# Kernel optimization log

Hardware: AMD Instinct MI355X
Metric: run time of the kernel (lower is better)

Reference implementation:

```python
import jax, jax.numpy as jnp
import numpy as np

B, S, D, H = 4, 2048, 1024, 16
DH = D // H


def setup_inputs() -> dict:
    key = jax.random.key(0)
    ks = jax.random.split(key, 5)
    scale = 0.02
    return {
        "in_features": jax.random.normal(ks[0], (B, S, D), dtype=jnp.float32),
        "Wq": jax.random.normal(ks[1], (D, D), dtype=jnp.float32) * scale,
        "Wk": jax.random.normal(ks[2], (D, D), dtype=jnp.float32) * scale,
        "Wv": jax.random.normal(ks[3], (D, D), dtype=jnp.float32) * scale,
        "Wo": jax.random.normal(ks[4], (D, D), dtype=jnp.float32) * scale,
    }


def reference(in_features, Wq, Wk, Wv, Wo):
    x = in_features  # [B, S, D]
    # projections: einsum '... s d_in, d_model d_in -> ... s d_model'  == x @ W.T
    q = jnp.einsum('bsd,md->bsm', x, Wq)
    k = jnp.einsum('bsd,md->bsm', x, Wk)
    v = jnp.einsum('bsd,md->bsm', x, Wv)
    # split heads: [B, H, S, DH]
    q = q.reshape(B, S, H, DH).transpose(0, 2, 1, 3)
    k = k.reshape(B, S, H, DH).transpose(0, 2, 1, 3)
    v = v.reshape(B, S, H, DH).transpose(0, 2, 1, 3)
    scale = 1.0 / jnp.sqrt(jnp.asarray(DH, dtype=q.dtype))
    scores = jnp.einsum('bhqd,bhkd->bhqk', q, k) * scale  # [B, H, S, S]
    causal = jnp.tril(jnp.ones((S, S), dtype=bool))
    scores = jnp.where(causal[None, None, :, :], scores, -jnp.inf)
    attn = jax.nn.softmax(scores, axis=-1)
    out = jnp.einsum('bhqk,bhkd->bhqd', attn, v)  # [B, H, S, DH]
    out = out.transpose(0, 2, 1, 3).reshape(B, S, D)
    # output projection: einsum '... s d_v, d_model d_v -> ... s d_model' == out @ Wo.T
    return jnp.einsum('bsd,md->bsm', out, Wo)
```

## Files before the change

kernel.cpp:

```cpp
#include <hip/hip_runtime.h>

typedef unsigned short u16;
typedef unsigned int u32;
typedef __attribute__((ext_vector_type(8))) short bf16x8;
typedef __attribute__((ext_vector_type(4))) short bf16x4;
typedef __attribute__((ext_vector_type(4))) float f32x4;

#define S_LEN 2048
#define NHEAD 16
#define DHEAD 64
#define DMODEL 1024

__device__ __forceinline__ u16 f2bf(float f) {
  unsigned u = __builtin_bit_cast(unsigned, f);
  unsigned r = (u + 0x7fffu + ((u >> 16) & 1u)) >> 16;
  return (u16)r;
}

__device__ __forceinline__ void gld_lds16(const void* g, void* l) {
  __builtin_amdgcn_global_load_lds((const __attribute__((address_space(1))) unsigned*)g,
                                   (__attribute__((address_space(3))) unsigned*)l,
                                   16, 0, 0);
}

__global__ void cast_all_kernel(const float* __restrict__ x,
                                const float* __restrict__ Wq, const float* __restrict__ Wk,
                                const float* __restrict__ Wv, const float* __restrict__ Wo,
                                u16* __restrict__ out) {
  int id = blockIdx.x * 256 + threadIdx.x;
  const float* s;
  int j;
  if (id < 2097152) {
    s = x; j = id;
  } else {
    int wid = id - 2097152;
    int wsel = wid >> 18;
    j = wid & 262143;
    s = wsel < 2 ? (wsel == 0 ? Wq : Wk) : (wsel == 2 ? Wv : Wo);
  }
  float4 v = reinterpret_cast<const float4*>(s)[j];
  ushort4 o;
  o.x = f2bf(v.x); o.y = f2bf(v.y); o.z = f2bf(v.z); o.w = f2bf(v.w);
  reinterpret_cast<ushort4*>(out)[id] = o;
}

__global__ __launch_bounds__(256) void gemm_qkv(const u16* __restrict__ A, const u16* __restrict__ Bw,
                                                u16* __restrict__ Qb) {
  __shared__ u16 smem[17408];
  u16* lA = smem;
  u16* lB = smem + 8192;
  const int hw = blockIdx.x;
  const int xcd = hw & 7, vv = hw >> 3;
  const int by = xcd * 8 + (vv & 7);
  const int bx = vv >> 3;
  const int tid = threadIdx.x;
  const int w = tid >> 6, lane = tid & 63;
  const int wm = w >> 1, wn = w & 1;
  const int c = lane & 15, qr = lane >> 4;
  const int brow = by * 128, bcol = bx * 128;
  const int sw = (qr ^ ((c >> 1) & 3)) * 8;
  f32x4 acc[4][4];
#pragma unroll
  for (int m = 0; m < 4; ++m)
#pragma unroll
    for (int n = 0; n < 4; ++n) acc[m][n] = (f32x4){0.f, 0.f, 0.f, 0.f};

  auto stage = [&](int kt, int bsel) {
    const int k0 = kt * 32;
#pragma unroll
    for (int i = 0; i < 2; ++i) {
      int slot = i * 256 + w * 64 + lane;
      int r = slot >> 2, sg = slot & 3;
      int sgs = sg ^ ((r >> 1) & 3);
      gld_lds16(A + (size_t)(brow + r) * DMODEL + k0 + sgs * 8, lA + bsel * 4096 + (i * 256 + w * 64) * 8);
      gld_lds16(Bw + (size_t)(bcol + r) * DMODEL + k0 + sgs * 8, lB + bsel * 4096 + (i * 256 + w * 64) * 8);
    }
  };

  stage(0, 0);
  __syncthreads();
  int cur = 0;
  for (int kt = 0; kt < 32; ++kt) {
    if (kt < 31) stage(kt + 1, cur ^ 1);
    bf16x8 af[4], bfr[4];
#pragma unroll
    for (int m = 0; m < 4; ++m) af[m] = *(const bf16x8*)(lA + cur * 4096 + (wm * 64 + m * 16 + c) * 32 + sw);
#pragma unroll
    for (int n = 0; n < 4; ++n) bfr[n] = *(const bf16x8*)(lB + cur * 4096 + (wn * 64 + n * 16 + c) * 32 + sw);
    __builtin_amdgcn_s_setprio(1);
#pragma unroll
    for (int m = 0; m < 4; ++m)
#pragma unroll
      for (int n = 0; n < 4; ++n)
        acc[m][n] = __builtin_amdgcn_mfma_f32_16x16x32_bf16(af[m], bfr[n], acc[m][n], 0, 0, 0);
    __builtin_amdgcn_s_setprio(0);
    __syncthreads();
    cur ^= 1;
  }

  u16* Kb = Qb + 8388608;
  u16* Vt = Kb + 8388608;
  const int mat = bcol >> 10;
  const int batch = by >> 4;
  const int sbase = brow & 2047;
  const int hbase = (bcol & 1023) >> 6;
  u16* ep = smem;

  if (mat == 2) {
#pragma unroll
    for (int mt = 0; mt < 4; ++mt)
#pragma unroll
      for (int nt = 0; nt < 4; ++nt) {
        int n = wn * 64 + nt * 16 + c;
        int m0 = wm * 64 + mt * 16 + qr * 4;
        ushort4 pk;
        pk.x = f2bf(acc[mt][nt][0]); pk.y = f2bf(acc[mt][nt][1]);
        pk.z = f2bf(acc[mt][nt][2]); pk.w = f2bf(acc[mt][nt][3]);
        *reinterpret_cast<ushort4*>(ep + n * 136 + m0) = pk;
      }
    __syncthreads();
#pragma unroll
    for (int i = 0; i < 8; ++i) {
      int id = i * 256 + tid;
      int n = id >> 4, mch = id & 15;
      int head = hbase + (n >> 6), dh = n & 63;
      uint4 v4 = *reinterpret_cast<const uint4*>(ep + n * 136 + mch * 8);
      *reinterpret_cast<uint4*>(Vt + ((size_t)(batch * NHEAD + head) * DHEAD + dh) * S_LEN + sbase + mch * 8) = v4;
    }
  } else {
    float scale = (mat == 0) ? 0.1803368801111204f : 1.0f;
    u16* dst = (mat == 0) ? Qb : Kb;
#pragma unroll
    for (int mt = 0; mt < 4; ++mt)
#pragma unroll
      for (int nt = 0; nt < 4; ++nt) {
        int n = wn * 64 + nt * 16 + c;
        int m0 = wm * 64 + mt * 16 + qr * 4;
#pragma unroll
        for (int r = 0; r < 4; ++r)
          ep[(m0 + r) * 136 + n] = f2bf(acc[mt][nt][r] * scale);
      }
    __syncthreads();
#pragma unroll
    for (int i = 0; i < 8; ++i) {
      int id = i * 256 + tid;
      int m = id >> 4, hh = (id >> 3) & 1, ch = id & 7;
      int head = hbase + hh;
      int s = sbase + m;
      uint4 v4 = *reinterpret_cast<const uint4*>(ep + m * 136 + hh * 64 + ch * 8);
      *reinterpret_cast<uint4*>(dst + ((size_t)(batch * NHEAD + head) * S_LEN + s) * DHEAD + ch * 8) = v4;
    }
  }
}

__global__ __launch_bounds__(256) void gemm_bt(const u16* __restrict__ A, const u16* __restrict__ Bw,
                                               float* __restrict__ outp) {
  __shared__ u16 lA[2][128 * 32];
  __shared__ u16 lB[2][128 * 32];
  const int hw = blockIdx.x;
  const int xcd = hw & 7, vv = hw >> 3;
  const int bx = vv >> 3, by = xcd * 8 + (vv & 7);
  const int tid = threadIdx.x;
  const int w = tid >> 6, lane = tid & 63;
  const int wm = w >> 1, wn = w & 1;
  const int c = lane & 15, qr = lane >> 4;
  const int brow = by * 128, bcol = bx * 128;
  const int sw = (qr ^ ((c >> 1) & 3)) * 8;
  f32x4 acc[4][4];
#pragma unroll
  for (int m = 0; m < 4; ++m)
#pragma unroll
    for (int n = 0; n < 4; ++n) acc[m][n] = (f32x4){0.f, 0.f, 0.f, 0.f};

  auto stage = [&](int kt, int bsel) {
    const int k0 = kt * 32;
#pragma unroll
    for (int i = 0; i < 2; ++i) {
      int slot = i * 256 + w * 64 + lane;
      int r = slot >> 2, sg = slot & 3;
      int sgs = sg ^ ((r >> 1) & 3);
      gld_lds16(A + (size_t)(brow + r) * DMODEL + k0 + sgs * 8, &lA[bsel][(i * 256 + w * 64) * 8]);
      gld_lds16(Bw + (size_t)(bcol + r) * DMODEL + k0 + sgs * 8, &lB[bsel][(i * 256 + w * 64) * 8]);
    }
  };

  stage(0, 0);
  __syncthreads();
  int cur = 0;
  for (int kt = 0; kt < 32; ++kt) {
    if (kt < 31) stage(kt + 1, cur ^ 1);
    bf16x8 af[4], bfr[4];
#pragma unroll
    for (int m = 0; m < 4; ++m) af[m] = *(const bf16x8*)(&lA[cur][(wm * 64 + m * 16 + c) * 32 + sw]);
#pragma unroll
    for (int n = 0; n < 4; ++n) bfr[n] = *(const bf16x8*)(&lB[cur][(wn * 64 + n * 16 + c) * 32 + sw]);
    __builtin_amdgcn_s_setprio(1);
#pragma unroll
    for (int m = 0; m < 4; ++m)
#pragma unroll
      for (int n = 0; n < 4; ++n)
        acc[m][n] = __builtin_amdgcn_mfma_f32_16x16x32_bf16(af[m], bfr[n], acc[m][n], 0, 0, 0);
    __builtin_amdgcn_s_setprio(0);
    __syncthreads();
    cur ^= 1;
  }

  const int rb = qr * 4;
#pragma unroll
  for (int m = 0; m < 4; ++m)
#pragma unroll
    for (int n = 0; n < 4; ++n) {
      f32x4 a = acc[m][n];
      int gm0 = brow + wm * 64 + m * 16 + rb;
      int gn = bcol + wn * 64 + n * 16 + c;
#pragma unroll
      for (int r = 0; r < 4; ++r) outp[(size_t)(gm0 + r) * DMODEL + gn] = a[r];
    }
}

__global__ __launch_bounds__(512, 4) void attn_kernel(const u16* __restrict__ Q, const u16* __restrict__ K,
                                                      const u16* __restrict__ Vt, u16* __restrict__ O) {
  __shared__ u16 lsK[2][64 * 64];
  __shared__ u16 lsV[2][64 * 64];
  __shared__ u16 lsP[8][16 * 64];
  const int x = blockIdx.x;
  const int xcd = x & 7, v = x >> 3;
  const int by = xcd * 8 + (v & 7);
  const int g = 15 - (v >> 3);
  const int tid = threadIdx.x;
  const int w = tid >> 6, lane = tid & 63;
  const int c = lane & 15, qr = lane >> 4;
  const int b = by >> 4, h = by & 15;
  u16* lp = lsP[w];

  const int q0 = g * 128 + w * 16;
  const int nd = 2 * g + (w >> 2);
  const int ntiles = 2 * g + 2;

  const u16* qrow = Q + ((size_t)by * S_LEN + q0 + c) * DHEAD;
  const bf16x8 aQ0 = *(const bf16x8*)(qrow + qr * 8);
  const bf16x8 aQ1 = *(const bf16x8*)(qrow + 32 + qr * 8);

  f32x4 o_acc[4];
#pragma unroll
  for (int d = 0; d < 4; ++d) o_acc[d] = (f32x4){0.f, 0.f, 0.f, 0.f};
  float l_run = 0.f;

  auto stage = [&](int kt, int bsel) {
    const int kv0 = kt * 64;
    int r = tid >> 3, p = tid & 7;
    int ps = p ^ (r & 7);
    gld_lds16(K + ((size_t)by * S_LEN + kv0 + r) * DHEAD + ps * 8, &lsK[bsel][(w * 64) * 8]);
    gld_lds16(Vt + ((size_t)by * DHEAD + r) * S_LEN + kv0 + ps * 8, &lsV[bsel][(w * 64) * 8]);
  };

  auto process = [&](const u16* bK, const u16* bV, int kt) {
    const int kv0 = kt * 64;
    f32x4 sc[4];
    __builtin_amdgcn_s_setprio(1);
#pragma unroll
    for (int nt = 0; nt < 4; ++nt) {
      int row = nt * 16 + c;
      const bf16x8 k0 = *(const bf16x8*)(bK + row * 64 + ((qr ^ (row & 7)) * 8));
      const bf16x8 k1 = *(const bf16x8*)(bK + row * 64 + (((4 + qr) ^ (row & 7)) * 8));
      f32x4 z = (f32x4){0.f, 0.f, 0.f, 0.f};
      z = __builtin_amdgcn_mfma_f32_16x16x32_bf16(k0, aQ0, z, 0, 0, 0);
      z = __builtin_amdgcn_mfma_f32_16x16x32_bf16(k1, aQ1, z, 0, 0, 0);
      sc[nt] = z;
    }
    __builtin_amdgcn_s_setprio(0);

    if (kt == nd) {
#pragma unroll
      for (int nt = 0; nt < 4; ++nt)
#pragma unroll
        for (int r = 0; r < 4; ++r) {
          int k_g = kv0 + nt * 16 + qr * 4 + r;
          int q_g = q0 + c;
          if (k_g > q_g) sc[nt][r] = -1e30f;
        }
    }

    float rs = 0.f;
#pragma unroll
    for (int nt = 0; nt < 4; ++nt) {
      float p0 = __builtin_amdgcn_exp2f(sc[nt][0]);
      float p1 = __builtin_amdgcn_exp2f(sc[nt][1]);
      float p2 = __builtin_amdgcn_exp2f(sc[nt][2]);
      float p3 = __builtin_amdgcn_exp2f(sc[nt][3]);
      rs += (p0 + p1) + (p2 + p3);
      u32 w01 = __builtin_amdgcn_perm(__builtin_bit_cast(u32, p1), __builtin_bit_cast(u32, p0), 0x07060302u);
      u32 w23 = __builtin_amdgcn_perm(__builtin_bit_cast(u32, p3), __builtin_bit_cast(u32, p2), 0x07060302u);
      uint2 pk; pk.x = w01; pk.y = w23;
      *reinterpret_cast<uint2*>(lp + c * 64 + (((nt * 4 + qr) ^ c) * 4)) = pk;
    }
    l_run += rs;

    bf16x8 pb[2];
#pragma unroll
    for (int ks = 0; ks < 2; ++ks) {
      bf16x4 lo = *(const bf16x4*)(lp + c * 64 + (((ks * 8 + qr * 2) ^ c) * 4));
      bf16x4 hi = *(const bf16x4*)(lp + c * 64 + (((ks * 8 + qr * 2 + 1) ^ c) * 4));
      pb[ks] = (bf16x8){lo[0], lo[1], lo[2], lo[3], hi[0], hi[1], hi[2], hi[3]};
    }
    __builtin_amdgcn_s_setprio(1);
#pragma unroll
    for (int dt = 0; dt < 4; ++dt) {
      int rowv = dt * 16 + c;
#pragma unroll
      for (int ks = 0; ks < 2; ++ks) {
        const bf16x8 vb = *(const bf16x8*)(bV + rowv * 64 + (((ks * 4 + qr) ^ (rowv & 7)) * 8));
        o_acc[dt] = __builtin_amdgcn_mfma_f32_16x16x32_bf16(vb, pb[ks], o_acc[dt], 0, 0, 0);
      }
    }
    __builtin_amdgcn_s_setprio(0);
  };

  stage(0, 0);
  __syncthreads();
  for (int kt = 0; kt < ntiles; kt += 2) {
    if (kt + 1 < ntiles) stage(kt + 1, 1);
    if (kt <= nd) process(lsK[0], lsV[0], kt);
    __syncthreads();
    if (kt + 2 < ntiles) stage(kt + 2, 0);
    if (kt + 1 <= nd) process(lsK[1], lsV[1], kt + 1);
    __syncthreads();
  }

  {
    l_run += __shfl_xor(l_run, 16);
    l_run += __shfl_xor(l_run, 32);
    float rl = 1.0f / l_run;
    int s = q0 + c;
#pragma unroll
    for (int dt = 0; dt < 4; ++dt) {
      ushort4 ok;
#pragma unroll
      for (int r = 0; r < 4; ++r) ((u16*)&ok)[r] = f2bf(o_acc[dt][r] * rl);
      *reinterpret_cast<ushort4*>(O + (((size_t)b * S_LEN + s) * NHEAD + h) * DHEAD + dt * 16 + qr * 4) = ok;
    }
  }
}

extern "C" void kernel_launch(void* const* d_in, const int* in_sizes, int n_in,
                              void* d_out, int out_size, void* d_ws, size_t ws_size,
                              hipStream_t stream) {
  (void)in_sizes; (void)n_in; (void)out_size; (void)ws_size;
  const float* x  = (const float*)d_in[0];
  const float* Wq = (const float*)d_in[1];
  const float* Wk = (const float*)d_in[2];
  const float* Wv = (const float*)d_in[3];
  const float* Wo = (const float*)d_in[4];

  u16* ws  = (u16*)d_ws;
  u16* xb  = ws;
  u16* wqb = xb  + 8388608;
  u16* wob = wqb + 3145728;
  u16* Qb  = wqb + 4194304;
  u16* Kb  = Qb  + 8388608;
  u16* Vt  = Kb  + 8388608;
  u16* Ob  = Vt  + 8388608;

  cast_all_kernel<<<12288, 256, 0, stream>>>(x, Wq, Wk, Wv, Wo, xb);

  gemm_qkv<<<1536, 256, 0, stream>>>(xb, wqb, Qb);
  attn_kernel<<<1024, 512, 0, stream>>>(Qb, Kb, Vt, Ob);
  gemm_bt<<<512, 256, 0, stream>>>(Ob, wob, (float*)d_out);
}
```

Baseline: 163.2 us.

## Process two query subtiles per wave in attention to reuse K/V fragments

Each attention wave now handles 32 query rows, as two 16-row subtiles, instead of 16, so each block covers 256 queries and the grid is halved. The K and V fragments read from LDS are reused across both subtiles, and the staged K/V tiles serve twice as many queries, which cuts LDS and global traffic per unit of work. The block-to-query-tile mapping is reordered for causal load balance. The cost is more registers per wave (accumulators, Q fragments and P buffers double), fewer blocks for load balancing, and a larger P LDS buffer, all of which may reduce occupancy.

```diff
diff --git a/kernel.cpp b/kernel.cpp
--- a/kernel.cpp
+++ b/kernel.cpp
@@ -222,95 +222,115 @@
                                                       const u16* __restrict__ Vt, u16* __restrict__ O) {
   __shared__ u16 lsK[2][64 * 64];
   __shared__ u16 lsV[2][64 * 64];
-  __shared__ u16 lsP[8][16 * 64];
+  __shared__ u16 lsP[8][2][16 * 64];
   const int x = blockIdx.x;
   const int xcd = x & 7, v = x >> 3;
   const int by = xcd * 8 + (v & 7);
-  const int g = 15 - (v >> 3);
+  const int p = v >> 3;
+  const int g = (p < 4) ? (7 - p) : (p - 4);
   const int tid = threadIdx.x;
   const int w = tid >> 6, lane = tid & 63;
   const int c = lane & 15, qr = lane >> 4;
   const int b = by >> 4, h = by & 15;
-  u16* lp = lsP[w];
-
-  const int q0 = g * 128 + w * 16;
-  const int nd = 2 * g + (w >> 2);
-  const int ntiles = 2 * g + 2;
-
-  const u16* qrow = Q + ((size_t)by * S_LEN + q0 + c) * DHEAD;
-  const bf16x8 aQ0 = *(const bf16x8*)(qrow + qr * 8);
-  const bf16x8 aQ1 = *(const bf16x8*)(qrow + 32 + qr * 8);
-
-  f32x4 o_acc[4];
-#pragma unroll
-  for (int d = 0; d < 4; ++d) o_acc[d] = (f32x4){0.f, 0.f, 0.f, 0.f};
-  float l_run = 0.f;
+
+  const int q0 = g * 256 + w * 32;
+  const int nd = 4 * g + (w >> 1);
+  const int ntiles = 4 * g + 4;
+
+  bf16x8 aQ[2][2];
+#pragma unroll
+  for (int qt = 0; qt < 2; ++qt)
+#pragma unroll
+    for (int ks = 0; ks < 2; ++ks)
+      aQ[qt][ks] = *(const bf16x8*)(Q + ((size_t)by * S_LEN + q0 + qt * 16 + c) * DHEAD + ks * 32 + qr * 8);
+
+  f32x4 o_acc[2][4];
+#pragma unroll
+  for (int qt = 0; qt < 2; ++qt)
+#pragma unroll
+    for (int d = 0; d < 4; ++d) o_acc[qt][d] = (f32x4){0.f, 0.f, 0.f, 0.f};
+  float l_run[2] = {0.f, 0.f};
 
   auto stage = [&](int kt, int bsel) {
     const int kv0 = kt * 64;
-    int r = tid >> 3, p = tid & 7;
-    int ps = p ^ (r & 7);
+    int r = tid >> 3, pp = tid & 7;
+    int ps = pp ^ (r & 7);
     gld_lds16(K + ((size_t)by * S_LEN + kv0 + r) * DHEAD + ps * 8, &lsK[bsel][(w * 64) * 8]);
     gld_lds16(Vt + ((size_t)by * DHEAD + r) * S_LEN + kv0 + ps * 8, &lsV[bsel][(w * 64) * 8]);
   };
 
   auto process = [&](const u16* bK, const u16* bV, int kt) {
     const int kv0 = kt * 64;
-    f32x4 sc[4];
+    f32x4 sc2[2][4];
     __builtin_amdgcn_s_setprio(1);
 #pragma unroll
     for (int nt = 0; nt < 4; ++nt) {
       int row = nt * 16 + c;
       const bf16x8 k0 = *(const bf16x8*)(bK + row * 64 + ((qr ^ (row & 7)) * 8));
       const bf16x8 k1 = *(const bf16x8*)(bK + row * 64 + (((4 + qr) ^ (row & 7)) * 8));
-      f32x4 z = (f32x4){0.f, 0.f, 0.f, 0.f};
-      z = __builtin_amdgcn_mfma_f32_16x16x32_bf16(k0, aQ0, z, 0, 0, 0);
-      z = __builtin_amdgcn_mfma_f32_16x16x32_bf16(k1, aQ1, z, 0, 0, 0);
-      sc[nt] = z;
+#pragma unroll
+      for (int qt = 0; qt < 2; ++qt) {
+        f32x4 z = (f32x4){0.f, 0.f, 0.f, 0.f};
+        z = __builtin_amdgcn_mfma_f32_16x16x32_bf16(k0, aQ[qt][0], z, 0, 0, 0);
+        z = __builtin_amdgcn_mfma_f32_16x16x32_bf16(k1, aQ[qt][1], z, 0, 0, 0);
+        sc2[qt][nt] = z;
+      }
     }
     __builtin_amdgcn_s_setprio(0);
 
     if (kt == nd) {
 #pragma unroll
-      for (int nt = 0; nt < 4; ++nt)
-#pragma unroll
-        for (int r = 0; r < 4; ++r) {
-          int k_g = kv0 + nt * 16 + qr * 4 + r;
-          int q_g = q0 + c;
-          if (k_g > q_g) sc[nt][r] = -1e30f;
-        }
-    }
-
-    float rs = 0.f;
-#pragma unroll
-    for (int nt = 0; nt < 4; ++nt) {
-      float p0 = __builtin_amdgcn_exp2f(sc[nt][0]);
-      float p1 = __builtin_amdgcn_exp2f(sc[nt][1]);
-      float p2 = __builtin_amdgcn_exp2f(sc[nt][2]);
-      float p3 = __builtin_amdgcn_exp2f(sc[nt][3]);
-      rs += (p0 + p1) + (p2 + p3);
-      u32 w01 = __builtin_amdgcn_perm(__builtin_bit_cast(u32, p1), __builtin_bit_cast(u32, p0), 0x07060302u);
-      u32 w23 = __builtin_amdgcn_perm(__builtin_bit_cast(u32, p3), __builtin_bit_cast(u32, p2), 0x07060302u);
-      uint2 pk; pk.x = w01; pk.y = w23;
-      *reinterpret_cast<uint2*>(lp + c * 64 + (((nt * 4 + qr) ^ c) * 4)) = pk;
-    }
-    l_run += rs;
-
-    bf16x8 pb[2];
-#pragma unroll
-    for (int ks = 0; ks < 2; ++ks) {
-      bf16x4 lo = *(const bf16x4*)(lp + c * 64 + (((ks * 8 + qr * 2) ^ c) * 4));
-      bf16x4 hi = *(const bf16x4*)(lp + c * 64 + (((ks * 8 + qr * 2 + 1) ^ c) * 4));
-      pb[ks] = (bf16x8){lo[0], lo[1], lo[2], lo[3], hi[0], hi[1], hi[2], hi[3]};
+      for (int qt = 0; qt < 2; ++qt)
+#pragma unroll
+        for (int nt = 0; nt < 4; ++nt)
+#pragma unroll
+          for (int r = 0; r < 4; ++r) {
+            int k_g = kv0 + nt * 16 + qr * 4 + r;
+            int q_g = q0 + qt * 16 + c;
+            if (k_g > q_g) sc2[qt][nt][r] = -1e30f;
+          }
+    }
+
+#pragma unroll
+    for (int qt = 0; qt < 2; ++qt) {
+      u16* lp = lsP[w][qt];
+      float rs = 0.f;
+#pragma unroll
+      for (int nt = 0; nt < 4; ++nt) {
+        float p0 = __builtin_amdgcn_exp2f(sc2[qt][nt][0]);
+        float p1 = __builtin_amdgcn_exp2f(sc2[qt][nt][1]);
+        float p2 = __builtin_amdgcn_exp2f(sc2[qt][nt][2]);
+        float p3 = __builtin_amdgcn_exp2f(sc2[qt][nt][3]);
+        rs += (p0 + p1) + (p2 + p3);
+        u32 w01 = __builtin_amdgcn_perm(__builtin_bit_cast(u32, p1), __builtin_bit_cast(u32, p0), 0x07060302u);
+        u32 w23 = __builtin_amdgcn_perm(__builtin_bit_cast(u32, p3), __builtin_bit_cast(u32, p2), 0x07060302u);
+        uint2 pk; pk.x = w01; pk.y = w23;
+        *reinterpret_cast<uint2*>(lp + c * 64 + (((nt * 4 + qr) ^ c) * 4)) = pk;
+      }
+      l_run[qt] += rs;
+    }
+
+    bf16x8 pb[2][2];
+#pragma unroll
+    for (int qt = 0; qt < 2; ++qt) {
+      u16* lp = lsP[w][qt];
+#pragma unroll
+      for (int ks = 0; ks < 2; ++ks) {
+        bf16x4 lo = *(const bf16x4*)(lp + c * 64 + (((ks * 8 + qr * 2) ^ c) * 4));
+        bf16x4 hi = *(const bf16x4*)(lp + c * 64 + (((ks * 8 + qr * 2 + 1) ^ c) * 4));
+        pb[qt][ks] = (bf16x8){lo[0], lo[1], lo[2], lo[3], hi[0], hi[1], hi[2], hi[3]};
+      }
     }
     __builtin_amdgcn_s_setprio(1);
 #pragma unroll
     for (int dt = 0; dt < 4; ++dt) {
       int rowv = dt * 16 + c;
-#pragma unroll
-      for (int ks = 0; ks < 2; ++ks) {
-        const bf16x8 vb = *(const bf16x8*)(bV + rowv * 64 + (((ks * 4 + qr) ^ (rowv & 7)) * 8));
-        o_acc[dt] = __builtin_amdgcn_mfma_f32_16x16x32_bf16(vb, pb[ks], o_acc[dt], 0, 0, 0);
+      const bf16x8 v0 = *(const bf16x8*)(bV + rowv * 64 + ((qr ^ (rowv & 7)) * 8));
+      const bf16x8 v1 = *(const bf16x8*)(bV + rowv * 64 + (((4 + qr) ^ (rowv & 7)) * 8));
+#pragma unroll
+      for (int qt = 0; qt < 2; ++qt) {
+        o_acc[qt][dt] = __builtin_amdgcn_mfma_f32_16x16x32_bf16(v0, pb[qt][0], o_acc[qt][dt], 0, 0, 0);
+        o_acc[qt][dt] = __builtin_amdgcn_mfma_f32_16x16x32_bf16(v1, pb[qt][1], o_acc[qt][dt], 0, 0, 0);
       }
     }
     __builtin_amdgcn_s_setprio(0);
@@ -327,16 +347,18 @@
     __syncthreads();
   }
 
-  {
-    l_run += __shfl_xor(l_run, 16);
-    l_run += __shfl_xor(l_run, 32);
-    float rl = 1.0f / l_run;
-    int s = q0 + c;
+#pragma unroll
+  for (int qt = 0; qt < 2; ++qt) {
+    float lr = l_run[qt];
+    lr += __shfl_xor(lr, 16);
+    lr += __shfl_xor(lr, 32);
+    float rl = 1.0f / lr;
+    int s = q0 + qt * 16 + c;
 #pragma unroll
     for (int dt = 0; dt < 4; ++dt) {
       ushort4 ok;
 #pragma unroll
-      for (int r = 0; r < 4; ++r) ((u16*)&ok)[r] = f2bf(o_acc[dt][r] * rl);
+      for (int r = 0; r < 4; ++r) ((u16*)&ok)[r] = f2bf(o_acc[qt][dt][r] * rl);
       *reinterpret_cast<ushort4*>(O + (((size_t)b * S_LEN + s) * NHEAD + h) * DHEAD + dt * 16 + qr * 4) = ok;
     }
   }
@@ -364,6 +386,6 @@
   cast_all_kernel<<<12288, 256, 0, stream>>>(x, Wq, Wk, Wv, Wo, xb);
 
   gemm_qkv<<<1536, 256, 0, stream>>>(xb, wqb, Qb);
-  attn_kernel<<<1024, 512, 0, stream>>>(Qb, Kb, Vt, Ob);
+  attn_kernel<<<512, 512, 0, stream>>>(Qb, Kb, Vt, Ob);
   gemm_bt<<<512, 256, 0, stream>>>(Ob, wob, (float*)d_out);
 }
```

New measurement: 168.7 us. +3.4%, slower.

## Triple-buffer K/V tiles and overlap next QK^T with current softmax-PV

Applied to the files above, without the earlier changes.

Splits the attention tile step into a QK^T stage and a softmax+PV stage, with K/V tiles kept in three shared-memory buffers. Each iteration computes the next tile's scores while finishing the current tile's softmax and PV, so there is one barrier per tile. The aim is to hide MFMA latency and exp/LDS work behind each other and keep loads two tiles ahead. In exchange, LDS per block grows by about a third and the carried score registers add register pressure, which may cut occupancy.

```diff
diff --git a/kernel.cpp b/kernel.cpp
--- a/kernel.cpp
+++ b/kernel.cpp
@@ -220,8 +220,8 @@
 
 __global__ __launch_bounds__(512, 4) void attn_kernel(const u16* __restrict__ Q, const u16* __restrict__ K,
                                                       const u16* __restrict__ Vt, u16* __restrict__ O) {
-  __shared__ u16 lsK[2][64 * 64];
-  __shared__ u16 lsV[2][64 * 64];
+  __shared__ u16 lsK[3][64 * 64];
+  __shared__ u16 lsV[3][64 * 64];
   __shared__ u16 lsP[8][16 * 64];
   const int x = blockIdx.x;
   const int xcd = x & 7, v = x >> 3;
@@ -246,17 +246,15 @@
   for (int d = 0; d < 4; ++d) o_acc[d] = (f32x4){0.f, 0.f, 0.f, 0.f};
   float l_run = 0.f;
 
-  auto stage = [&](int kt, int bsel) {
+  auto stage = [&](int kt, u16* dK, u16* dV) {
     const int kv0 = kt * 64;
     int r = tid >> 3, p = tid & 7;
     int ps = p ^ (r & 7);
-    gld_lds16(K + ((size_t)by * S_LEN + kv0 + r) * DHEAD + ps * 8, &lsK[bsel][(w * 64) * 8]);
-    gld_lds16(Vt + ((size_t)by * DHEAD + r) * S_LEN + kv0 + ps * 8, &lsV[bsel][(w * 64) * 8]);
-  };
-
-  auto process = [&](const u16* bK, const u16* bV, int kt) {
-    const int kv0 = kt * 64;
-    f32x4 sc[4];
+    gld_lds16(K + ((size_t)by * S_LEN + kv0 + r) * DHEAD + ps * 8, dK + (w * 64) * 8);
+    gld_lds16(Vt + ((size_t)by * DHEAD + r) * S_LEN + kv0 + ps * 8, dV + (w * 64) * 8);
+  };
+
+  auto qk = [&](const u16* bK, f32x4* sc) {
     __builtin_amdgcn_s_setprio(1);
 #pragma unroll
     for (int nt = 0; nt < 4; ++nt) {
@@ -269,7 +267,10 @@
       sc[nt] = z;
     }
     __builtin_amdgcn_s_setprio(0);
-
+  };
+
+  auto smpv = [&](const u16* bV, f32x4* sc, int kt) {
+    const int kv0 = kt * 64;
     if (kt == nd) {
 #pragma unroll
       for (int nt = 0; nt < 4; ++nt)
@@ -280,7 +281,6 @@
           if (k_g > q_g) sc[nt][r] = -1e30f;
         }
     }
-
     float rs = 0.f;
 #pragma unroll
     for (int nt = 0; nt < 4; ++nt) {
@@ -316,15 +316,25 @@
     __builtin_amdgcn_s_setprio(0);
   };
 
-  stage(0, 0);
+  u16 *K0 = lsK[0], *K1 = lsK[1], *K2 = lsK[2];
+  u16 *V0 = lsV[0], *V1 = lsV[1], *V2 = lsV[2];
+  f32x4 scA[4], scB[4];
+
+  stage(0, K0, V0);
+  stage(1, K1, V1);
   __syncthreads();
-  for (int kt = 0; kt < ntiles; kt += 2) {
-    if (kt + 1 < ntiles) stage(kt + 1, 1);
-    if (kt <= nd) process(lsK[0], lsV[0], kt);
-    __syncthreads();
-    if (kt + 2 < ntiles) stage(kt + 2, 0);
-    if (kt + 1 <= nd) process(lsK[1], lsV[1], kt + 1);
-    __syncthreads();
+  qk(K0, scA);
+
+#pragma unroll 1
+  for (int t = 0; t < ntiles; ++t) {
+    if (t + 2 < ntiles) stage(t + 2, K2, V2);
+    if (t + 1 <= nd) qk(K1, scB);
+    if (t <= nd) smpv(V0, scA, t);
+    __syncthreads();
+    u16* tk = K0; K0 = K1; K1 = K2; K2 = tk;
+    u16* tv = V0; V0 = V1; V1 = V2; V2 = tv;
+#pragma unroll
+    for (int i = 0; i < 4; ++i) scA[i] = scB[i];
   }
 
   {
```

Result: slower. 169.0 us (+3.5%).

## Triple-buffer K/V tiles in attention with explicit vmcnt waits

Applied to the files above, without the earlier changes.

The attention kernel's K/V shared-memory staging goes from double to triple buffering, so loads run two tiles ahead of compute. Explicit s_waitcnt vmcnt counters and raw s_barrier calls replace __syncthreads, so each tile waits only for its own async global-to-LDS loads rather than draining all outstanding memory operations. The aim is to hide global load latency behind the MFMA work. The cost is more LDS per block, which may lower occupancy, and the hand-set vmcnt values depend on how many loads stage() issues.

```diff
diff --git a/kernel.cpp b/kernel.cpp
--- a/kernel.cpp
+++ b/kernel.cpp
@@ -218,10 +218,17 @@
     }
 }
 
+#define AVM(N) do { __builtin_amdgcn_sched_barrier(0);                                       \
+  asm volatile("s_waitcnt vmcnt(" #N ")" ::: "memory");                                      \
+  __builtin_amdgcn_sched_barrier(0); } while (0)
+#define ABAR do { __builtin_amdgcn_sched_barrier(0);                                         \
+  __builtin_amdgcn_s_barrier();                                                              \
+  __builtin_amdgcn_sched_barrier(0); } while (0)
+
 __global__ __launch_bounds__(512, 4) void attn_kernel(const u16* __restrict__ Q, const u16* __restrict__ K,
                                                       const u16* __restrict__ Vt, u16* __restrict__ O) {
-  __shared__ u16 lsK[2][64 * 64];
-  __shared__ u16 lsV[2][64 * 64];
+  __shared__ u16 lsK[3][64 * 64];
+  __shared__ u16 lsV[3][64 * 64];
   __shared__ u16 lsP[8][16 * 64];
   const int x = blockIdx.x;
   const int xcd = x & 7, v = x >> 3;
@@ -317,15 +324,27 @@
   };
 
   stage(0, 0);
-  __syncthreads();
-  for (int kt = 0; kt < ntiles; kt += 2) {
-    if (kt + 1 < ntiles) stage(kt + 1, 1);
-    if (kt <= nd) process(lsK[0], lsV[0], kt);
-    __syncthreads();
-    if (kt + 2 < ntiles) stage(kt + 2, 0);
-    if (kt + 1 <= nd) process(lsK[1], lsV[1], kt + 1);
-    __syncthreads();
-  }
+  stage(1, 1);
+
+  int t = 0, bt = 0;
+#pragma unroll 1
+  for (; t + 2 < ntiles; ++t) {
+    int b2 = bt + 2; if (b2 >= 3) b2 -= 3;
+    stage(t + 2, b2);
+    AVM(4);
+    ABAR;
+    if (t <= nd) process(lsK[bt], lsV[bt], t);
+    ABAR;
+    ++bt; if (bt == 3) bt = 0;
+  }
+  AVM(2);
+  ABAR;
+  if (t <= nd) process(lsK[bt], lsV[bt], t);
+  ABAR;
+  ++t; ++bt; if (bt == 3) bt = 0;
+  AVM(0);
+  ABAR;
+  if (t <= nd) process(lsK[bt], lsV[bt], t);
 
   {
     l_run += __shfl_xor(l_run, 16);
```

Result: no change. 164.0 us (+0.5%).
